# Optimization experiments

Hardware: AMD Instinct MI355X
Metric: run time of the kernel (lower is better)

Reference implementation:

```python
import jax, jax.numpy as jnp
import numpy as np

WIN = 5            # LNCC window_size
W_IMG = 1.0        # image_loss_weight
W_SMOOTH = 0.02    # smoothness_weight
W_JAC = 0.01       # jacobian_weight
W_INV = 0.1        # inverse_consistency_weight
EPS = 1e-05


def _avg_pool3d(x, k):
    # matches F.avg_pool3d(kernel=k, stride=1, padding=k//2, count_include_pad=True)
    p = k // 2
    s = jax.lax.reduce_window(x, jnp.array(0.0, x.dtype), jax.lax.add,
                              (1, 1, k, k, k), (1, 1, 1, 1, 1),
                              [(0, 0), (0, 0), (p, p), (p, p), (p, p)])
    return s / (k ** 3)


def _lncc(source, target):
    conv = lambda v: _avg_pool3d(v, WIN)
    sm, tm = conv(source), conv(target)
    sv = conv(source * source) - sm * sm
    tv = conv(target * target) - tm * tm
    cross = conv(source * target) - sm * tm
    lncc = cross * cross / (sv * tv + EPS)
    return jnp.nan_to_num(1.0 - lncc.mean(), nan=1.0, posinf=1.0, neginf=1.0)


def _grad3d_l2(disp):
    # Grad3D(penalty='l2'): mean squared forward differences per axis
    dz = disp[:, :, 1:] - disp[:, :, :-1]
    dy = disp[:, :, :, 1:] - disp[:, :, :, :-1]
    dx = disp[:, :, :, :, 1:] - disp[:, :, :, :, :-1]
    return (jnp.mean(dz * dz) + jnp.mean(dy * dy) + jnp.mean(dx * dx)) / 3.0


def _neg_jacobian(d):
    dx = d[:, :, 1:, :-1, :-1] - d[:, :, :-1, :-1, :-1]
    dy = d[:, :, :-1, 1:, :-1] - d[:, :, :-1, :-1, :-1]
    dz = d[:, :, :-1, :-1, 1:] - d[:, :, :-1, :-1, :-1]
    a00, a01, a02 = 1.0 + dx[:, 0], dy[:, 0], dz[:, 0]
    a10, a11, a12 = dx[:, 1], 1.0 + dy[:, 1], dz[:, 1]
    a20, a21, a22 = dx[:, 2], dy[:, 2], 1.0 + dz[:, 2]
    det = (a00 * (a11 * a22 - a12 * a21)
           - a01 * (a10 * a22 - a12 * a20)
           + a02 * (a10 * a21 - a11 * a20))
    det = jnp.nan_to_num(det, nan=0.0, posinf=1000.0, neginf=-1000.0)
    return jnp.mean(jax.nn.relu(-det))


def _warp(vol, flow):
    # SpatialTransformer: trilinear sample of vol at identity_grid + flow,
    # coordinates clamped to volume borders. vol [B,C,D,H,W], flow [B,3,D,H,W].
    B, C, D, H, W = vol.shape
    zz, yy, xx = jnp.meshgrid(jnp.arange(D, dtype=vol.dtype),
                              jnp.arange(H, dtype=vol.dtype),
                              jnp.arange(W, dtype=vol.dtype), indexing='ij')
    cz = jnp.clip(zz[None] + flow[:, 0], 0.0, D - 1)
    cy = jnp.clip(yy[None] + flow[:, 1], 0.0, H - 1)
    cx = jnp.clip(xx[None] + flow[:, 2], 0.0, W - 1)
    z0 = jnp.floor(cz); y0 = jnp.floor(cy); x0 = jnp.floor(cx)
    fz, fy, fx = cz - z0, cy - y0, cx - x0
    z0i = z0.astype(jnp.int32); y0i = y0.astype(jnp.int32); x0i = x0.astype(jnp.int32)
    z1i = jnp.minimum(z0i + 1, D - 1)
    y1i = jnp.minimum(y0i + 1, H - 1)
    x1i = jnp.minimum(x0i + 1, W - 1)
    volf = vol.reshape(B, C, D * H * W)

    def gather(zi, yi, xi):
        idx = ((zi * H + yi) * W + xi).reshape(B, 1, -1)
        idx = jnp.broadcast_to(idx, (B, C, idx.shape[-1]))
        return jnp.take_along_axis(volf, idx, axis=2).reshape(B, C, D, H, W)

    fz_, fy_, fx_ = fz[:, None], fy[:, None], fx[:, None]
    c000 = gather(z0i, y0i, x0i); c001 = gather(z0i, y0i, x1i)
    c010 = gather(z0i, y1i, x0i); c011 = gather(z0i, y1i, x1i)
    c100 = gather(z1i, y0i, x0i); c101 = gather(z1i, y0i, x1i)
    c110 = gather(z1i, y1i, x0i); c111 = gather(z1i, y1i, x1i)
    c00 = c000 * (1 - fx_) + c001 * fx_
    c01 = c010 * (1 - fx_) + c011 * fx_
    c10 = c100 * (1 - fx_) + c101 * fx_
    c11 = c110 * (1 - fx_) + c111 * fx_
    c0 = c00 * (1 - fy_) + c01 * fy_
    c1 = c10 * (1 - fy_) + c11 * fy_
    return c0 * (1 - fz_) + c1 * fz_


def _inverse_consistency(fwd, bwd):
    composed = fwd + _warp(bwd, fwd)
    return jnp.nan_to_num(jnp.mean(composed * composed), nan=0.0, posinf=1000.0, neginf=0.0)


def setup_inputs() -> dict:
    key = jax.random.key(0)
    k1, k2, k3, k4 = jax.random.split(key, 4)
    shp_img = (1, 1, 128, 128, 128)
    shp_disp = (1, 3, 128, 128, 128)
    return {
        'source': jax.random.normal(k1, shp_img, dtype=jnp.float32),
        'target': jax.random.normal(k2, shp_img, dtype=jnp.float32),
        'forward_disp': jax.random.normal(k3, shp_disp, dtype=jnp.float32),
        'backward_disp': jax.random.normal(k4, shp_disp, dtype=jnp.float32),
    }


def reference(source, target, forward_disp, backward_disp):
    total = (W_IMG * _lncc(source, target)
             + W_SMOOTH * _grad3d_l2(forward_disp)
             + W_JAC * _neg_jacobian(forward_disp)
             + W_INV * _inverse_consistency(forward_disp, backward_disp))
    return total
```

## Files before the change

kernel.cpp:

```cpp
#include <hip/hip_runtime.h>
#include <hip/hip_fp16.h>
#include <math.h>

#define DD 128
#define HH 128
#define WW 128
#define NN (DD*HH*WW)
#define DJ 127

#define NB_LNCC 4096
#define NB_FUSED 8192
#define LOFF 0
#define GOFF (NB_LNCC)
#define JOFF (NB_LNCC + NB_FUSED)
#define IOFF (NB_LNCC + 2*NB_FUSED)
#define NSLOTS (NB_LNCC + 3*NB_FUSED)
#define BWDH_OFF ((size_t)((NSLOTS * 8 + 255) & ~255))
#define WS_NEED (BWDH_OFF + (size_t)NN * 8)

struct __align__(8) Half4 { __half x, y, z, w; };

__device__ __forceinline__ double wave_reduce(double v) {
    #pragma unroll
    for (int o = 32; o > 0; o >>= 1) v += __shfl_down(v, o);
    return v;
}

template <int NWAVES>
__device__ __forceinline__ double block_reduce(double v, double* red, int tid) {
    v = wave_reduce(v);
    int wid = tid >> 6, lane = tid & 63;
    __syncthreads();
    if (lane == 0) red[wid] = v;
    __syncthreads();
    double x = 0.0;
    if (tid == 0) {
        #pragma unroll
        for (int w = 0; w < NWAVES; w++) x += red[w];
    }
    return x;
}

__device__ __forceinline__ float4 add4(float4 a, float4 b) {
    return make_float4(a.x + b.x, a.y + b.y, a.z + b.z, a.w + b.w);
}

__device__ __forceinline__ float jac_term(const float* dz_, const float* dy_, const float* dx_) {
    float a00 = 1.f + dz_[0], a01 = dy_[0], a02 = dx_[0];
    float a10 = dz_[1], a11 = 1.f + dy_[1], a12 = dx_[1];
    float a20 = dz_[2], a21 = dy_[2], a22 = 1.f + dx_[2];
    float det = a00 * (a11 * a22 - a12 * a21)
              - a01 * (a10 * a22 - a12 * a20)
              + a02 * (a10 * a21 - a11 * a20);
    if (isnan(det)) det = 0.f;
    else if (isinf(det)) det = det > 0.f ? 1000.f : -1000.f;
    float neg = -det;
    return neg > 0.f ? neg : 0.f;
}

__global__ __launch_bounds__(256) void interleave4h_kernel(const float* __restrict__ bwd,
                                                           Half4* __restrict__ bwdh) {
    const int i4 = (blockIdx.x * 256 + threadIdx.x) * 4;
    float4 b0 = *(const float4*)(bwd + i4);
    float4 b1 = *(const float4*)(bwd + NN + i4);
    float4 b2 = *(const float4*)(bwd + 2 * NN + i4);
    Half4 o0 = { __float2half(b0.x), __float2half(b1.x), __float2half(b2.x), __float2half(0.f) };
    Half4 o1 = { __float2half(b0.y), __float2half(b1.y), __float2half(b2.y), __float2half(0.f) };
    Half4 o2 = { __float2half(b0.z), __float2half(b1.z), __float2half(b2.z), __float2half(0.f) };
    Half4 o3 = { __float2half(b0.w), __float2half(b1.w), __float2half(b2.w), __float2half(0.f) };
    bwdh[i4 + 0] = o0;
    bwdh[i4 + 1] = o1;
    bwdh[i4 + 2] = o2;
    bwdh[i4 + 3] = o3;
}

__global__ __launch_bounds__(512) void lncc_kernel(const float* __restrict__ src,
                                                   const float* __restrict__ tgt,
                                                   double* __restrict__ ws) {
    __shared__ __align__(16) float F1[5][12 * 12 * 8];
    __shared__ __align__(16) float F2[5][12 * 8 * 8];
    __shared__ double red[8];
    const int tid = threadIdx.x;
    const int slot = (blockIdx.x & 7) * 512 + (blockIdx.x >> 3);
    const int bz = (slot >> 8) * 8;
    const int by = ((slot >> 4) & 15) * 8;
    const int bx = (slot & 15) * 8;

    if (tid < 288) {
        const int h = tid & 1;
        const int row = tid >> 1;
        const int ly = row % 12, lz = row / 12;
        const int gy = by + ly - 2, gz = bz + lz - 2;
        const bool rowok = (gy >= 0 && gy < HH && gz >= 0 && gz < DD);
        const int rowbase = (gz * HH + gy) * WW;
        const int w0 = bx + h * 4 - 4;

        float4 lsv[3], ltv[3];
        #pragma unroll
        for (int p = 0; p < 3; p++) {
            int gx = w0 + 4 * p;
            if (rowok && gx >= 0 && gx <= WW - 4) {
                lsv[p] = *(const float4*)(src + rowbase + gx);
                ltv[p] = *(const float4*)(tgt + rowbase + gx);
            } else {
                lsv[p] = make_float4(0.f, 0.f, 0.f, 0.f);
                ltv[p] = make_float4(0.f, 0.f, 0.f, 0.f);
            }
        }
        const float* ls = (const float*)lsv;
        const float* lt = (const float*)ltv;

        float o[5][4];
        #pragma unroll
        for (int k = 0; k < 4; k++) {
            float s1 = 0.f, t1s = 0.f, s2 = 0.f, t2s = 0.f, st = 0.f;
            #pragma unroll
            for (int d = 0; d < 5; d++) {
                float a = ls[k + d + 2], b = lt[k + d + 2];
                s1 += a; t1s += b;
                s2 = fmaf(a, a, s2); t2s = fmaf(b, b, t2s); st = fmaf(a, b, st);
            }
            o[0][k] = s1; o[1][k] = t1s; o[2][k] = s2; o[3][k] = t2s; o[4][k] = st;
        }
        const int obase = (lz * 12 + ly) * 8 + h * 4;
        #pragma unroll
        for (int f = 0; f < 5; f++)
            *(float4*)&F1[f][obase] = make_float4(o[f][0], o[f][1], o[f][2], o[f][3]);
    }
    __syncthreads();

    if (tid < 192) {
        const int h = tid & 1;
        const int r = tid >> 1;
        const int oy = r & 7, lz = r >> 3;
        float4 a0 = make_float4(0.f, 0.f, 0.f, 0.f), a1 = a0, a2 = a0, a3 = a0, a4 = a0;
        #pragma unroll
        for (int dy = 0; dy < 5; dy++) {
            const int j = (lz * 12 + oy + dy) * 8 + h * 4;
            a0 = add4(a0, *(const float4*)&F1[0][j]);
            a1 = add4(a1, *(const float4*)&F1[1][j]);
            a2 = add4(a2, *(const float4*)&F1[2][j]);
            a3 = add4(a3, *(const float4*)&F1[3][j]);
            a4 = add4(a4, *(const float4*)&F1[4][j]);
        }
        const int jo = (lz * 8 + oy) * 8 + h * 4;
        *(float4*)&F2[0][jo] = a0;
        *(float4*)&F2[1][jo] = a1;
        *(float4*)&F2[2][jo] = a2;
        *(float4*)&F2[3][jo] = a3;
        *(float4*)&F2[4][jo] = a4;
    }
    __syncthreads();

    double lsum = 0.0;
    if (tid < 128) {
        const int h = tid & 1;
        const int r = tid >> 1;
        const int oy = r & 7, oz = r >> 3;
        float A[5][4];
        #pragma unroll
        for (int f = 0; f < 5; f++) { A[f][0] = A[f][1] = A[f][2] = A[f][3] = 0.f; }
        #pragma unroll
        for (int dz = 0; dz < 5; dz++) {
            const int j = ((oz + dz) * 8 + oy) * 8 + h * 4;
            #pragma unroll
            for (int f = 0; f < 5; f++) {
                float4 q = *(const float4*)&F2[f][j];
                A[f][0] += q.x; A[f][1] += q.y; A[f][2] += q.z; A[f][3] += q.w;
            }
        }
        const float inv125 = 1.f / 125.f;
        #pragma unroll
        for (int k = 0; k < 4; k++) {
            float sm = A[0][k] * inv125, tm = A[1][k] * inv125;
            float sv = A[2][k] * inv125 - sm * sm;
            float tv = A[3][k] * inv125 - tm * tm;
            float cross = A[4][k] * inv125 - sm * tm;
            float l = cross * cross / (sv * tv + 1e-5f);
            lsum += (double)l;
        }
    }
    double tot = block_reduce<8>(lsum, red, tid);
    if (tid == 0) ws[LOFF + slot] = tot;
}

__global__ __launch_bounds__(256, 4) void fused1h_kernel(const float* __restrict__ fwd,
                                                         const Half4* __restrict__ bwdh,
                                                         double* __restrict__ ws) {
    __shared__ double red[4];

    const int swz = (blockIdx.x & 7) * (NB_FUSED / 8) + (blockIdx.x >> 3);
    const int idx = swz * 256 + threadIdx.x;
    const int x = idx & 127; const int y = (idx >> 7) & 127; const int z = idx >> 14;
    const bool hx = (x < WW - 1), hy = (y < HH - 1), hz = (z < DD - 1);

    double accG = 0.0, accJ = 0.0, accI = 0.0;

    float v[3], ddx[3], ddy[3], ddz[3];
    #pragma unroll
    for (int c = 0; c < 3; c++) {
        const float* p = fwd + c * NN + idx;
        float vv = p[0];
        v[c]   = vv;
        ddx[c] = hx ? (p[1] - vv) : 0.f;
        ddy[c] = hy ? (p[WW] - vv) : 0.f;
        ddz[c] = hz ? (p[HH * WW] - vv) : 0.f;
    }

    {
        float g = 0.f;
        #pragma unroll
        for (int c = 0; c < 3; c++)
            g = fmaf(ddz[c], ddz[c], fmaf(ddy[c], ddy[c], fmaf(ddx[c], ddx[c], g)));
        accG = (double)g;
    }

    if (hx && hy && hz) accJ = (double)jac_term(ddz, ddy, ddx);

    {
        float cz = fminf(fmaxf((float)z + v[0], 0.f), (float)(DD - 1));
        float cy = fminf(fmaxf((float)y + v[1], 0.f), (float)(HH - 1));
        float cx = fminf(fmaxf((float)x + v[2], 0.f), (float)(WW - 1));
        float z0f = floorf(cz), y0f = floorf(cy), x0f = floorf(cx);
        float fz = cz - z0f, fy = cy - y0f, fx = cx - x0f;
        int z0 = (int)z0f, y0 = (int)y0f, x0 = (int)x0f;
        int z1 = min(z0 + 1, DD - 1), y1 = min(y0 + 1, HH - 1), x1 = min(x0 + 1, WW - 1);
        int b00 = (z0 * HH + y0) * WW, b01 = (z0 * HH + y1) * WW;
        int b10 = (z1 * HH + y0) * WW, b11 = (z1 * HH + y1) * WW;
        Half4 H000 = bwdh[b00 + x0], H001 = bwdh[b00 + x1];
        Half4 H010 = bwdh[b01 + x0], H011 = bwdh[b01 + x1];
        Half4 H100 = bwdh[b10 + x0], H101 = bwdh[b10 + x1];
        Half4 H110 = bwdh[b11 + x0], H111 = bwdh[b11 + x1];
        float w000 = (1.f - fz) * (1.f - fy) * (1.f - fx);
        float w001 = (1.f - fz) * (1.f - fy) * fx;
        float w010 = (1.f - fz) * fy * (1.f - fx);
        float w011 = (1.f - fz) * fy * fx;
        float w100 = fz * (1.f - fy) * (1.f - fx);
        float w101 = fz * (1.f - fy) * fx;
        float w110 = fz * fy * (1.f - fx);
        float w111 = fz * fy * fx;
        float c0 = v[0] + w000 * __half2float(H000.x) + w001 * __half2float(H001.x)
                        + w010 * __half2float(H010.x) + w011 * __half2float(H011.x)
                        + w100 * __half2float(H100.x) + w101 * __half2float(H101.x)
                        + w110 * __half2float(H110.x) + w111 * __half2float(H111.x);
        float c1 = v[1] + w000 * __half2float(H000.y) + w001 * __half2float(H001.y)
                        + w010 * __half2float(H010.y) + w011 * __half2float(H011.y)
                        + w100 * __half2float(H100.y) + w101 * __half2float(H101.y)
                        + w110 * __half2float(H110.y) + w111 * __half2float(H111.y);
        float c2 = v[2] + w000 * __half2float(H000.z) + w001 * __half2float(H001.z)
                        + w010 * __half2float(H010.z) + w011 * __half2float(H011.z)
                        + w100 * __half2float(H100.z) + w101 * __half2float(H101.z)
                        + w110 * __half2float(H110.z) + w111 * __half2float(H111.z);
        accI = (double)(c0 * c0 + c1 * c1 + c2 * c2);
    }

    double tG = block_reduce<4>(accG, red, threadIdx.x);
    double tJ = block_reduce<4>(accJ, red, threadIdx.x);
    double tI = block_reduce<4>(accI, red, threadIdx.x);
    if (threadIdx.x == 0) {
        ws[GOFF + swz] = tG;
        ws[JOFF + swz] = tJ;
        ws[IOFF + swz] = tI;
    }
}

__global__ __launch_bounds__(256) void fused_fallback(const float* __restrict__ fwd,
                                                      const float* __restrict__ bwd,
                                                      double* __restrict__ ws) {
    __shared__ double red[4];
    const int idx = blockIdx.x * 256 + threadIdx.x;
    const int x = idx & 127; const int y = (idx >> 7) & 127; const int z = idx >> 14;
    const bool hx = (x < WW - 1), hy = (y < HH - 1), hz = (z < DD - 1);

    double accG = 0.0, accJ = 0.0, accI = 0.0;
    float v[3], ddx[3], ddy[3], ddz[3];
    #pragma unroll
    for (int c = 0; c < 3; c++) {
        const float* p = fwd + c * NN + idx;
        float vv = p[0];
        v[c]   = vv;
        ddx[c] = hx ? (p[1] - vv) : 0.f;
        ddy[c] = hy ? (p[WW] - vv) : 0.f;
        ddz[c] = hz ? (p[HH * WW] - vv) : 0.f;
    }
    float g = 0.f;
    #pragma unroll
    for (int c = 0; c < 3; c++)
        g = fmaf(ddz[c], ddz[c], fmaf(ddy[c], ddy[c], fmaf(ddx[c], ddx[c], g)));
    accG = (double)g;
    if (hx && hy && hz) accJ = (double)jac_term(ddz, ddy, ddx);
    {
        float cz = fminf(fmaxf((float)z + v[0], 0.f), (float)(DD - 1));
        float cy = fminf(fmaxf((float)y + v[1], 0.f), (float)(HH - 1));
        float cx = fminf(fmaxf((float)x + v[2], 0.f), (float)(WW - 1));
        float z0f = floorf(cz), y0f = floorf(cy), x0f = floorf(cx);
        float fz = cz - z0f, fy = cy - y0f, fx = cx - x0f;
        int z0 = (int)z0f, y0 = (int)y0f, x0 = (int)x0f;
        int z1 = min(z0 + 1, DD - 1), y1 = min(y0 + 1, HH - 1), x1 = min(x0 + 1, WW - 1);
        int i000 = (z0 * HH + y0) * WW + x0, i001 = (z0 * HH + y0) * WW + x1;
        int i010 = (z0 * HH + y1) * WW + x0, i011 = (z0 * HH + y1) * WW + x1;
        int i100 = (z1 * HH + y0) * WW + x0, i101 = (z1 * HH + y0) * WW + x1;
        int i110 = (z1 * HH + y1) * WW + x0, i111 = (z1 * HH + y1) * WW + x1;
        float w000 = (1.f - fz) * (1.f - fy) * (1.f - fx);
        float w001 = (1.f - fz) * (1.f - fy) * fx;
        float w010 = (1.f - fz) * fy * (1.f - fx);
        float w011 = (1.f - fz) * fy * fx;
        float w100 = fz * (1.f - fy) * (1.f - fx);
        float w101 = fz * (1.f - fy) * fx;
        float w110 = fz * fy * (1.f - fx);
        float w111 = fz * fy * fx;
        #pragma unroll
        for (int c = 0; c < 3; c++) {
            const float* b = bwd + c * NN;
            float warped = w000 * b[i000] + w001 * b[i001]
                         + w010 * b[i010] + w011 * b[i011]
                         + w100 * b[i100] + w101 * b[i101]
                         + w110 * b[i110] + w111 * b[i111];
            float comp = v[c] + warped;
            accI += (double)(comp * comp);
        }
    }

    double tG = block_reduce<4>(accG, red, threadIdx.x);
    double tJ = block_reduce<4>(accJ, red, threadIdx.x);
    double tI = block_reduce<4>(accI, red, threadIdx.x);
    if (threadIdx.x == 0) {
        ws[GOFF + blockIdx.x] = tG;
        ws[JOFF + blockIdx.x] = tJ;
        ws[IOFF + blockIdx.x] = tI;
    }
}

__global__ __launch_bounds__(256) void finalize_kernel(const double* __restrict__ ws,
                                                       float* __restrict__ out) {
    __shared__ double red[4];
    double l = 0.0, g = 0.0, j = 0.0, inv = 0.0;
    for (int k = threadIdx.x; k < NB_LNCC; k += 256) l += ws[LOFF + k];
    for (int k = threadIdx.x; k < NB_FUSED; k += 256) {
        g   += ws[GOFF + k];
        j   += ws[JOFF + k];
        inv += ws[IOFF + k];
    }
    double tl = block_reduce<4>(l, red, threadIdx.x);
    double tg = block_reduce<4>(g, red, threadIdx.x);
    double tj = block_reduce<4>(j, red, threadIdx.x);
    double ti = block_reduce<4>(inv, red, threadIdx.x);
    if (threadIdx.x == 0) {
        double li = 1.0 - tl / (double)NN;
        if (isnan(li) || isinf(li)) li = 1.0;
        double grad = tg / (9.0 * 127.0 * 128.0 * 128.0);
        double jac  = tj / ((double)DJ * DJ * DJ);
        double iv = ti / (3.0 * (double)NN);
        if (isnan(iv)) iv = 0.0;
        else if (isinf(iv)) iv = iv > 0.0 ? 1000.0 : 0.0;
        out[0] = (float)(1.0 * li + 0.02 * grad + 0.01 * jac + 0.1 * iv);
    }
}

extern "C" void kernel_launch(void* const* d_in, const int* in_sizes, int n_in,
                              void* d_out, int out_size, void* d_ws, size_t ws_size,
                              hipStream_t stream) {
    const float* src = (const float*)d_in[0];
    const float* tgt = (const float*)d_in[1];
    const float* fwd = (const float*)d_in[2];
    const float* bwd = (const float*)d_in[3];
    double* ws = (double*)d_ws;
    float* out = (float*)d_out;

    if (ws_size >= WS_NEED) {
        Half4* bwdh = (Half4*)((char*)d_ws + BWDH_OFF);
        interleave4h_kernel<<<2048, 256, 0, stream>>>(bwd, bwdh);
        lncc_kernel<<<4096, 512, 0, stream>>>(src, tgt, ws);
        fused1h_kernel<<<NB_FUSED, 256, 0, stream>>>(fwd, bwdh, ws);
    } else {
        lncc_kernel<<<4096, 512, 0, stream>>>(src, tgt, ws);
        fused_fallback<<<NB_FUSED, 256, 0, stream>>>(fwd, bwd, ws);
    }
    finalize_kernel<<<1, 256, 0, stream>>>(ws, out);
}
```

Measured before the change: 90.63 us.

## Store LNCC box-filter partial sums in fp16 shared memory and halve block size

The LNCC kernel now keeps its intermediate y- and z-pass box sums in shared memory as packed half2 values instead of fp32, and accumulates them with __hadd2. The block shrinks from 512 to 256 threads, each final thread handling two outputs. This cuts the shared-memory footprint and LDS traffic and lets all threads take part in the last stage. The cost is precision: sums of squares over 125 voxels held in fp16 lose accuracy, and variance computed by cancellation can be badly wrong. That could push the loss past tolerance.

```diff
diff --git a/kernel.cpp b/kernel.cpp
--- a/kernel.cpp
+++ b/kernel.cpp
@@ -18,7 +18,9 @@
 #define BWDH_OFF ((size_t)((NSLOTS * 8 + 255) & ~255))
 #define WS_NEED (BWDH_OFF + (size_t)NN * 8)
 
-struct __align__(8) Half4 { __half x, y, z, w; };
+struct __align__(8)  Half4 { __half x, y, z, w; };
+struct __align__(16) H8  { __half2 a0, b0, a1, b1; };
+struct __align__(8)  HS4 { __half2 u, v; };
 
 __device__ __forceinline__ double wave_reduce(double v) {
     #pragma unroll
@@ -39,10 +41,6 @@
         for (int w = 0; w < NWAVES; w++) x += red[w];
     }
     return x;
-}
-
-__device__ __forceinline__ float4 add4(float4 a, float4 b) {
-    return make_float4(a.x + b.x, a.y + b.y, a.z + b.z, a.w + b.w);
 }
 
 __device__ __forceinline__ float jac_term(const float* dz_, const float* dy_, const float* dx_) {
@@ -56,6 +54,15 @@
     else if (isinf(det)) det = det > 0.f ? 1000.f : -1000.f;
     float neg = -det;
     return neg > 0.f ? neg : 0.f;
+}
+
+__device__ __forceinline__ float lncc_val(float S1, float T1, float S2, float T2, float ST) {
+    const float inv125 = 1.f / 125.f;
+    float sm = S1 * inv125, tm = T1 * inv125;
+    float sv = S2 * inv125 - sm * sm;
+    float tv = T2 * inv125 - tm * tm;
+    float cross = ST * inv125 - sm * tm;
+    return cross * cross / (sv * tv + 1e-5f);
 }
 
 __global__ __launch_bounds__(256) void interleave4h_kernel(const float* __restrict__ bwd,
@@ -74,21 +81,23 @@
     bwdh[i4 + 3] = o3;
 }
 
-__global__ __launch_bounds__(512) void lncc_kernel(const float* __restrict__ src,
+__global__ __launch_bounds__(256) void lncc_kernel(const float* __restrict__ src,
                                                    const float* __restrict__ tgt,
                                                    double* __restrict__ ws) {
-    __shared__ __align__(16) float F1[5][12 * 12 * 8];
-    __shared__ __align__(16) float F2[5][12 * 8 * 8];
-    __shared__ double red[8];
+    __shared__ H8  F1A[576];
+    __shared__ HS4 F1S[288];
+    __shared__ H8  F2A[384];
+    __shared__ HS4 F2S[192];
+    __shared__ double red[4];
     const int tid = threadIdx.x;
     const int slot = (blockIdx.x & 7) * 512 + (blockIdx.x >> 3);
     const int bz = (slot >> 8) * 8;
     const int by = ((slot >> 4) & 15) * 8;
     const int bx = (slot & 15) * 8;
 
-    if (tid < 288) {
-        const int h = tid & 1;
-        const int row = tid >> 1;
+    for (int t = tid; t < 288; t += 256) {
+        const int h = t & 1;
+        const int row = t >> 1;
         const int ly = row % 12, lz = row / 12;
         const int gy = by + ly - 2, gz = bz + lz - 2;
         const bool rowok = (gy >= 0 && gy < HH && gz >= 0 && gz < DD);
@@ -123,9 +132,14 @@
             o[0][k] = s1; o[1][k] = t1s; o[2][k] = s2; o[3][k] = t2s; o[4][k] = st;
         }
         const int obase = (lz * 12 + ly) * 8 + h * 4;
-        #pragma unroll
-        for (int f = 0; f < 5; f++)
-            *(float4*)&F1[f][obase] = make_float4(o[f][0], o[f][1], o[f][2], o[f][3]);
+        H8 e0 = { __floats2half2_rn(o[0][0], o[1][0]), __floats2half2_rn(o[2][0], o[3][0]),
+                  __floats2half2_rn(o[0][1], o[1][1]), __floats2half2_rn(o[2][1], o[3][1]) };
+        H8 e1 = { __floats2half2_rn(o[0][2], o[1][2]), __floats2half2_rn(o[2][2], o[3][2]),
+                  __floats2half2_rn(o[0][3], o[1][3]), __floats2half2_rn(o[2][3], o[3][3]) };
+        F1A[(obase >> 1) + 0] = e0;
+        F1A[(obase >> 1) + 1] = e1;
+        HS4 es = { __floats2half2_rn(o[4][0], o[4][1]), __floats2half2_rn(o[4][2], o[4][3]) };
+        F1S[obase >> 2] = es;
     }
     __syncthreads();
 
@@ -133,54 +147,56 @@
         const int h = tid & 1;
         const int r = tid >> 1;
         const int oy = r & 7, lz = r >> 3;
-        float4 a0 = make_float4(0.f, 0.f, 0.f, 0.f), a1 = a0, a2 = a0, a3 = a0, a4 = a0;
+        const __half2 z2 = __float2half2_rn(0.f);
+        __half2 A0 = z2, B0 = z2, A1 = z2, B1 = z2;
+        __half2 A2 = z2, B2 = z2, A3 = z2, B3 = z2;
+        __half2 S01 = z2, S23 = z2;
         #pragma unroll
         for (int dy = 0; dy < 5; dy++) {
-            const int j = (lz * 12 + oy + dy) * 8 + h * 4;
-            a0 = add4(a0, *(const float4*)&F1[0][j]);
-            a1 = add4(a1, *(const float4*)&F1[1][j]);
-            a2 = add4(a2, *(const float4*)&F1[2][j]);
-            a3 = add4(a3, *(const float4*)&F1[3][j]);
-            a4 = add4(a4, *(const float4*)&F1[4][j]);
+            const int jb = (lz * 12 + oy + dy) * 8 + h * 4;
+            H8 p = F1A[(jb >> 1) + 0];
+            H8 q = F1A[(jb >> 1) + 1];
+            A0 = __hadd2(A0, p.a0); B0 = __hadd2(B0, p.b0);
+            A1 = __hadd2(A1, p.a1); B1 = __hadd2(B1, p.b1);
+            A2 = __hadd2(A2, q.a0); B2 = __hadd2(B2, q.b0);
+            A3 = __hadd2(A3, q.a1); B3 = __hadd2(B3, q.b1);
+            HS4 s = F1S[jb >> 2];
+            S01 = __hadd2(S01, s.u); S23 = __hadd2(S23, s.v);
         }
         const int jo = (lz * 8 + oy) * 8 + h * 4;
-        *(float4*)&F2[0][jo] = a0;
-        *(float4*)&F2[1][jo] = a1;
-        *(float4*)&F2[2][jo] = a2;
-        *(float4*)&F2[3][jo] = a3;
-        *(float4*)&F2[4][jo] = a4;
+        H8 w0v = { A0, B0, A1, B1 };
+        H8 w1v = { A2, B2, A3, B3 };
+        F2A[(jo >> 1) + 0] = w0v;
+        F2A[(jo >> 1) + 1] = w1v;
+        HS4 wsv = { S01, S23 };
+        F2S[jo >> 2] = wsv;
     }
     __syncthreads();
 
     double lsum = 0.0;
-    if (tid < 128) {
-        const int h = tid & 1;
-        const int r = tid >> 1;
-        const int oy = r & 7, oz = r >> 3;
-        float A[5][4];
-        #pragma unroll
-        for (int f = 0; f < 5; f++) { A[f][0] = A[f][1] = A[f][2] = A[f][3] = 0.f; }
+    {
+        const int pos = tid * 2;
+        const int oz = pos >> 6, oy = (pos >> 3) & 7, ox = pos & 7;
+        const __half2 z2 = __float2half2_rn(0.f);
+        __half2 cA0 = z2, cB0 = z2, cA1 = z2, cB1 = z2, cS = z2;
         #pragma unroll
         for (int dz = 0; dz < 5; dz++) {
-            const int j = ((oz + dz) * 8 + oy) * 8 + h * 4;
-            #pragma unroll
-            for (int f = 0; f < 5; f++) {
-                float4 q = *(const float4*)&F2[f][j];
-                A[f][0] += q.x; A[f][1] += q.y; A[f][2] += q.z; A[f][3] += q.w;
-            }
-        }
-        const float inv125 = 1.f / 125.f;
-        #pragma unroll
-        for (int k = 0; k < 4; k++) {
-            float sm = A[0][k] * inv125, tm = A[1][k] * inv125;
-            float sv = A[2][k] * inv125 - sm * sm;
-            float tv = A[3][k] * inv125 - tm * tm;
-            float cross = A[4][k] * inv125 - sm * tm;
-            float l = cross * cross / (sv * tv + 1e-5f);
-            lsum += (double)l;
-        }
-    }
-    double tot = block_reduce<8>(lsum, red, tid);
+            const int j = (((oz + dz) * 8 + oy) * 8) + ox;
+            H8 p = F2A[j >> 1];
+            cA0 = __hadd2(cA0, p.a0); cB0 = __hadd2(cB0, p.b0);
+            cA1 = __hadd2(cA1, p.a1); cB1 = __hadd2(cB1, p.b1);
+            HS4 s = F2S[j >> 2];
+            cS = __hadd2(cS, (j & 2) ? s.v : s.u);
+        }
+        float2 s1t1_0 = __half22float2(cA0);
+        float2 s2t2_0 = __half22float2(cB0);
+        float2 s1t1_1 = __half22float2(cA1);
+        float2 s2t2_1 = __half22float2(cB1);
+        float2 stp    = __half22float2(cS);
+        lsum = (double)lncc_val(s1t1_0.x, s1t1_0.y, s2t2_0.x, s2t2_0.y, stp.x)
+             + (double)lncc_val(s1t1_1.x, s1t1_1.y, s2t2_1.x, s2t2_1.y, stp.y);
+    }
+    double tot = block_reduce<4>(lsum, red, tid);
     if (tid == 0) ws[LOFF + slot] = tot;
 }
 
@@ -370,10 +386,10 @@
     if (ws_size >= WS_NEED) {
         Half4* bwdh = (Half4*)((char*)d_ws + BWDH_OFF);
         interleave4h_kernel<<<2048, 256, 0, stream>>>(bwd, bwdh);
-        lncc_kernel<<<4096, 512, 0, stream>>>(src, tgt, ws);
+        lncc_kernel<<<4096, 256, 0, stream>>>(src, tgt, ws);
         fused1h_kernel<<<NB_FUSED, 256, 0, stream>>>(fwd, bwdh, ws);
     } else {
-        lncc_kernel<<<4096, 512, 0, stream>>>(src, tgt, ws);
+        lncc_kernel<<<4096, 256, 0, stream>>>(src, tgt, ws);
         fused_fallback<<<NB_FUSED, 256, 0, stream>>>(fwd, bwd, ws);
     }
     finalize_kernel<<<1, 256, 0, stream>>>(ws, out);
```

Result: faster. 83.35 us (-8.0%).
